# Optimization experiments

Measured on AMD Instinct MI355X. Metric: run time of the kernel, lower is better.

Reference implementation:

```python
import jax, jax.numpy as jnp
import numpy as np

B, N, FIN, FOUT, H = 8, 1024, 256, 256, 4
D = FOUT // H  # head_dim = 64
LN_EPS = 1e-5
NEG_INF = -1e9


def setup_inputs() -> dict:
    key = jax.random.key(0)
    k_x, k_adj, k_w, k_a = jax.random.split(key, 4)
    x = jax.random.normal(k_x, (B, N, FIN), dtype=jnp.float32)
    # sparse binary adjacency with self-loops (dense mask, as the module expects)
    adj = (jax.random.uniform(k_adj, (B, N, N)) < 0.05).astype(jnp.float32)
    adj = jnp.maximum(adj, jnp.eye(N, dtype=jnp.float32)[None])
    W = jax.random.normal(k_w, (FIN, FOUT), dtype=jnp.float32) * 0.02
    gamma = jnp.ones((FOUT,), dtype=jnp.float32)
    beta = jnp.zeros((FOUT,), dtype=jnp.float32)
    a = jax.random.normal(k_a, (2 * D,), dtype=jnp.float32) * 0.02
    return {"x": x, "adj_matrix": adj, "W": W, "gamma": gamma, "beta": beta, "a": a}


def reference(x, adj_matrix, W, gamma, beta, a):
    # h = LayerNorm(x @ W)
    h = jnp.einsum("bnf,fo->bno", x, W)
    mu = jnp.mean(h, axis=-1, keepdims=True)
    var = jnp.mean(jnp.square(h - mu), axis=-1, keepdims=True)
    h = (h - mu) * jax.lax.rsqrt(var + LN_EPS) * gamma + beta
    h = h.reshape(B, N, H, D)
    # a^T [h_i ; h_j] == a_src . h_i + a_dst . h_j  (exact decomposition of the
    # concat+Linear(2D->1) attention score, avoiding the O(B*N^2*H*2D) concat)
    a_src, a_dst = a[:D], a[D:]
    e_i = jnp.einsum("bnhd,d->bnh", h, a_src)  # term for node i (query)
    e_j = jnp.einsum("bnhd,d->bnh", h, a_dst)  # term for node j (key)
    e = e_i[:, :, None, :] + e_j[:, None, :, :]  # [B, N_i, N_j, H]
    e = jnp.where(e > 0, e, 0.2 * e)  # LeakyReLU(0.2)
    e = jnp.where(adj_matrix[..., None] == 0, NEG_INF, e)
    alpha = jax.nn.softmax(e, axis=2)  # softmax over neighbors j
    # dropout is identity in eval/reference mode
    h_out = jnp.einsum("bijh,bjhd->bihd", alpha, h)
    return h_out.reshape(B, N, FOUT)
```

## Files before the change

### kernel.cpp

```cpp
#include <hip/hip_runtime.h>
#include <hip/hip_bf16.h>

#define BB 8
#define NN 1024
#define FIN 256
#define FOUT 256
#define NH 4
#define DD 64
#define CAP 192

typedef short short8 __attribute__((ext_vector_type(8)));
typedef short short4v __attribute__((ext_vector_type(4)));
typedef float floatx4 __attribute__((ext_vector_type(4)));

__device__ __forceinline__ short f2bf(float f) {
    unsigned int u = __builtin_bit_cast(unsigned int, f);
    unsigned int r = (u + 0x7fffu + ((u >> 16) & 1u)) >> 16;
    return (short)r;
}

__global__ __launch_bounds__(256) void k_gemm(const float* __restrict__ x,
                                              const float* __restrict__ W,
                                              float* __restrict__ h) {
    __shared__ short As[64 * 40];
    __shared__ short Bt[64 * 40];
    const int m0 = blockIdx.x * 64;
    const int n0 = blockIdx.y * 64;
    const int t = threadIdx.x;
    const int w = t >> 6;
    const int lane = t & 63;
    const int quad = lane >> 4;
    const int l15 = lane & 15;

    floatx4 acc[4];
#pragma unroll
    for (int nt = 0; nt < 4; ++nt) acc[nt] = (floatx4)0.f;

    const int bn = t & 63;
    const int bkg = t >> 6;

    for (int k0 = 0; k0 < FIN; k0 += 32) {
#pragma unroll
        for (int q = 0; q < 2; ++q) {
            int lin = t * 4 + q * 1024;
            int m = lin >> 5, k = lin & 31;
            float4 v = *(const float4*)&x[(size_t)(m0 + m) * FIN + k0 + k];
            short4v s;
            s.x = f2bf(v.x); s.y = f2bf(v.y); s.z = f2bf(v.z); s.w = f2bf(v.w);
            *(short4v*)&As[m * 40 + k] = s;
        }
        {
            float f[8];
#pragma unroll
            for (int kk = 0; kk < 8; ++kk)
                f[kk] = W[(size_t)(k0 + bkg * 8 + kk) * FOUT + n0 + bn];
            short4v s0, s1;
            s0.x = f2bf(f[0]); s0.y = f2bf(f[1]); s0.z = f2bf(f[2]); s0.w = f2bf(f[3]);
            s1.x = f2bf(f[4]); s1.y = f2bf(f[5]); s1.z = f2bf(f[6]); s1.w = f2bf(f[7]);
            *(short4v*)&Bt[bn * 40 + bkg * 8]     = s0;
            *(short4v*)&Bt[bn * 40 + bkg * 8 + 4] = s1;
        }
        __syncthreads();
        short8 a = *(short8*)&As[(w * 16 + l15) * 40 + quad * 8];
#pragma unroll
        for (int nt = 0; nt < 4; ++nt) {
            short8 b = *(short8*)&Bt[(nt * 16 + l15) * 40 + quad * 8];
            acc[nt] = __builtin_amdgcn_mfma_f32_16x16x32_bf16(a, b, acc[nt], 0, 0, 0);
        }
        __syncthreads();
    }
#pragma unroll
    for (int nt = 0; nt < 4; ++nt)
#pragma unroll
        for (int reg = 0; reg < 4; ++reg)
            h[(size_t)(m0 + w * 16 + quad * 4 + reg) * FOUT + n0 + nt * 16 + l15] = acc[nt][reg];
}

__global__ __launch_bounds__(256) void k_ln(float* __restrict__ h,
                                            const float* __restrict__ gamma,
                                            const float* __restrict__ beta,
                                            const float* __restrict__ a,
                                            float* __restrict__ e_src,
                                            float* __restrict__ e_dst) {
    const int row = blockIdx.x;
    const int t = threadIdx.x;
    const size_t base = (size_t)row * FOUT;
    const int wave = t >> 6, lane = t & 63;
    __shared__ float red[8];

    float v = h[base + t];
    float s = v;
#pragma unroll
    for (int off = 32; off; off >>= 1) s += __shfl_xor(s, off);
    if (lane == 0) red[wave] = s;
    __syncthreads();
    float mean = (red[0] + red[1] + red[2] + red[3]) * (1.0f / 256.0f);
    float dv = v - mean;
    float q = dv * dv;
#pragma unroll
    for (int off = 32; off; off >>= 1) q += __shfl_xor(q, off);
    if (lane == 0) red[4 + wave] = q;
    __syncthreads();
    float var = (red[4] + red[5] + red[6] + red[7]) * (1.0f / 256.0f);
    float hn = dv * rsqrtf(var + 1e-5f) * gamma[t] + beta[t];
    h[base + t] = hn;

    float ps = hn * a[lane];
    float pd = hn * a[64 + lane];
#pragma unroll
    for (int off = 32; off; off >>= 1) {
        ps += __shfl_xor(ps, off);
        pd += __shfl_xor(pd, off);
    }
    if (lane == 0) {
        e_src[row * NH + wave] = ps;
        e_dst[row * NH + wave] = pd;
    }
}

__global__ __launch_bounds__(256) void k_attn(const float* __restrict__ h,
                                              const float* __restrict__ adj,
                                              const float* __restrict__ e_src,
                                              const float* __restrict__ e_dst,
                                              float* __restrict__ out) {
    __shared__ int cnt;
    __shared__ int jlist[CAP];
    __shared__ float4 wsl[CAP];
    __shared__ float accs[4][4][64];
    __shared__ float Ss[4][64];

    const int b = blockIdx.y;
    const int i = blockIdx.x;
    const int t = threadIdx.x;
    const float* hp   = h   + (size_t)b * NN * FOUT;
    const float* adjp = adj + ((size_t)b * NN + i) * NN;
    const float* edp  = e_dst + (size_t)b * NN * NH;

    const float4 esv = *(const float4*)&e_src[((size_t)b * NN + i) * NH];

    if (t == 0) cnt = 0;
    __syncthreads();

    float4 av = *(const float4*)&adjp[t * 4];
    float am[4] = {av.x, av.y, av.z, av.w};
#pragma unroll
    for (int q = 0; q < 4; ++q) {
        if (am[q] != 0.0f) {
            int j = t * 4 + q;
            int pos = atomicAdd(&cnt, 1);
            float4 ed = *(const float4*)&edp[(size_t)j * NH];
            float e0 = esv.x + ed.x, e1 = esv.y + ed.y, e2 = esv.z + ed.z, e3 = esv.w + ed.w;
            e0 = e0 > 0.f ? e0 : 0.2f * e0;
            e1 = e1 > 0.f ? e1 : 0.2f * e1;
            e2 = e2 > 0.f ? e2 : 0.2f * e2;
            e3 = e3 > 0.f ? e3 : 0.2f * e3;
            float4 w4;
            w4.x = __expf(e0); w4.y = __expf(e1); w4.z = __expf(e2); w4.w = __expf(e3);
            jlist[pos] = j;
            wsl[pos] = w4;
        }
    }
    __syncthreads();

    const int n = cnt;
    const int fg = t & 63;
    const int hh = fg >> 4;
    const int w = t >> 6;

    float4 acc = make_float4(0.f, 0.f, 0.f, 0.f);
    float S = 0.f;
    int p = w;
    while (p + 12 < n) {
        int jj[4]; float wv[4]; float4 hv[4];
#pragma unroll
        for (int q = 0; q < 4; ++q) jj[q] = jlist[p + q * 4];
#pragma unroll
        for (int q = 0; q < 4; ++q) {
            wv[q] = ((const float*)&wsl[p + q * 4])[hh];
            hv[q] = *(const float4*)&hp[(size_t)jj[q] * FOUT + fg * 4];
        }
#pragma unroll
        for (int q = 0; q < 4; ++q) {
            acc.x = fmaf(wv[q], hv[q].x, acc.x);
            acc.y = fmaf(wv[q], hv[q].y, acc.y);
            acc.z = fmaf(wv[q], hv[q].z, acc.z);
            acc.w = fmaf(wv[q], hv[q].w, acc.w);
            S += wv[q];
        }
        p += 16;
    }
    for (; p < n; p += 4) {
        int j = jlist[p];
        float wv = ((const float*)&wsl[p])[hh];
        float4 hv = *(const float4*)&hp[(size_t)j * FOUT + fg * 4];
        acc.x = fmaf(wv, hv.x, acc.x);
        acc.y = fmaf(wv, hv.y, acc.y);
        acc.z = fmaf(wv, hv.z, acc.z);
        acc.w = fmaf(wv, hv.w, acc.w);
        S += wv;
    }
    accs[w][0][fg] = acc.x; accs[w][1][fg] = acc.y;
    accs[w][2][fg] = acc.z; accs[w][3][fg] = acc.w;
    Ss[w][fg] = S;
    __syncthreads();

    if (t < 64) {
        float4 o = make_float4(0.f, 0.f, 0.f, 0.f);
        float St = 0.f;
#pragma unroll
        for (int q = 0; q < 4; ++q) {
            o.x += accs[q][0][t]; o.y += accs[q][1][t];
            o.z += accs[q][2][t]; o.w += accs[q][3][t];
            St += Ss[q][t];
        }
        float inv = 1.0f / St;
        o.x *= inv; o.y *= inv; o.z *= inv; o.w *= inv;
        *(float4*)&out[((size_t)b * NN + i) * FOUT + t * 4] = o;
    }
}

extern "C" void kernel_launch(void* const* d_in, const int* in_sizes, int n_in,
                              void* d_out, int out_size, void* d_ws, size_t ws_size,
                              hipStream_t stream) {
    const float* x     = (const float*)d_in[0];
    const float* adj   = (const float*)d_in[1];
    const float* W     = (const float*)d_in[2];
    const float* gamma = (const float*)d_in[3];
    const float* beta  = (const float*)d_in[4];
    const float* a     = (const float*)d_in[5];
    float* out = (float*)d_out;

    float* h     = (float*)d_ws;
    float* e_src = h + (size_t)BB * NN * FOUT;
    float* e_dst = e_src + (size_t)BB * NN * NH;

    k_gemm<<<dim3(128, 4), 256, 0, stream>>>(x, W, h);
    k_ln<<<dim3(BB * NN), 256, 0, stream>>>(h, gamma, beta, a, e_src, e_dst);
    k_attn<<<dim3(NN, BB), 256, 0, stream>>>(h, adj, e_src, e_dst, out);
}
```

Baseline: 128.5 us.

## Fuse GEMM with LayerNorm, store h as bf16, aggregate neighbor atomics per wave

Replaces the separate GEMM and LayerNorm kernels with one kernel that computes a 16-row tile against a pre-transposed bf16 W, applies LayerNorm and the attention score dot products in registers, and writes h as bf16. The attention kernel gathers bf16 neighbor rows, halving gather bytes. Per-element shared atomics become one ballot-based atomic per wave. Storing h in bf16 reduces precision of the aggregated output, and a small extra kernel transposes W each call.

```diff
diff --git a/kernel.cpp b/kernel.cpp
--- a/kernel.cpp
+++ b/kernel.cpp
@@ -6,7 +6,6 @@
 #define FIN 256
 #define FOUT 256
 #define NH 4
-#define DD 64
 #define CAP 192
 
 typedef short short8 __attribute__((ext_vector_type(8)));
@@ -18,107 +17,147 @@
     unsigned int r = (u + 0x7fffu + ((u >> 16) & 1u)) >> 16;
     return (short)r;
 }
-
-__global__ __launch_bounds__(256) void k_gemm(const float* __restrict__ x,
-                                              const float* __restrict__ W,
-                                              float* __restrict__ h) {
-    __shared__ short As[64 * 40];
-    __shared__ short Bt[64 * 40];
-    const int m0 = blockIdx.x * 64;
-    const int n0 = blockIdx.y * 64;
+__device__ __forceinline__ float bf2f(unsigned short s) {
+    return __builtin_bit_cast(float, (unsigned int)s << 16);
+}
+
+__global__ __launch_bounds__(256) void k_wt(const float* __restrict__ W,
+                                            unsigned short* __restrict__ Wt) {
+    __shared__ unsigned short ts[64][80];
+    const int k0 = blockIdx.x * 64, n0 = blockIdx.y * 64;
     const int t = threadIdx.x;
-    const int w = t >> 6;
-    const int lane = t & 63;
-    const int quad = lane >> 4;
-    const int l15 = lane & 15;
+#pragma unroll
+    for (int q = 0; q < 4; ++q) {
+        int lin = t + q * 256;
+        int r = lin >> 4, c4 = lin & 15;
+        float4 v = *(const float4*)&W[(size_t)(k0 + r) * FOUT + n0 + c4 * 4];
+        ts[c4 * 4 + 0][r] = (unsigned short)f2bf(v.x);
+        ts[c4 * 4 + 1][r] = (unsigned short)f2bf(v.y);
+        ts[c4 * 4 + 2][r] = (unsigned short)f2bf(v.z);
+        ts[c4 * 4 + 3][r] = (unsigned short)f2bf(v.w);
+    }
+    __syncthreads();
+#pragma unroll
+    for (int q = 0; q < 2; ++q) {
+        int lin = t + q * 256;
+        int row = lin >> 3, kg = lin & 7;
+        short8 s = *(short8*)&ts[row][kg * 8];
+        *(short8*)&Wt[(size_t)(n0 + row) * FIN + k0 + kg * 8] = s;
+    }
+}
+
+__global__ __launch_bounds__(256) void k_gemm_ln(const float* __restrict__ x,
+                                                 const unsigned short* __restrict__ Wt,
+                                                 const float* __restrict__ gamma,
+                                                 const float* __restrict__ beta,
+                                                 const float* __restrict__ a,
+                                                 unsigned short* __restrict__ hb,
+                                                 float* __restrict__ e_src,
+                                                 float* __restrict__ e_dst) {
+    __shared__ unsigned short As[16 * 264];
+    __shared__ float sumL[4][16], sqL[4][16];
+    const int m0 = blockIdx.x * 16;
+    const int t = threadIdx.x;
+    const int w = t >> 6, lane = t & 63, quad = lane >> 4, l15 = lane & 15;
+
+#pragma unroll
+    for (int q = 0; q < 4; ++q) {
+        int lin = t + q * 256;
+        int row = lin >> 6, c4 = lin & 63;
+        float4 v = *(const float4*)&x[(size_t)(m0 + row) * FIN + c4 * 4];
+        short4v s;
+        s.x = f2bf(v.x); s.y = f2bf(v.y); s.z = f2bf(v.z); s.w = f2bf(v.w);
+        *(short4v*)&As[row * 264 + c4 * 4] = s;
+    }
+    __syncthreads();
 
     floatx4 acc[4];
 #pragma unroll
     for (int nt = 0; nt < 4; ++nt) acc[nt] = (floatx4)0.f;
 
-    const int bn = t & 63;
-    const int bkg = t >> 6;
-
-    for (int k0 = 0; k0 < FIN; k0 += 32) {
-#pragma unroll
-        for (int q = 0; q < 2; ++q) {
-            int lin = t * 4 + q * 1024;
-            int m = lin >> 5, k = lin & 31;
-            float4 v = *(const float4*)&x[(size_t)(m0 + m) * FIN + k0 + k];
-            short4v s;
-            s.x = f2bf(v.x); s.y = f2bf(v.y); s.z = f2bf(v.z); s.w = f2bf(v.w);
-            *(short4v*)&As[m * 40 + k] = s;
-        }
-        {
-            float f[8];
-#pragma unroll
-            for (int kk = 0; kk < 8; ++kk)
-                f[kk] = W[(size_t)(k0 + bkg * 8 + kk) * FOUT + n0 + bn];
-            short4v s0, s1;
-            s0.x = f2bf(f[0]); s0.y = f2bf(f[1]); s0.z = f2bf(f[2]); s0.w = f2bf(f[3]);
-            s1.x = f2bf(f[4]); s1.y = f2bf(f[5]); s1.z = f2bf(f[6]); s1.w = f2bf(f[7]);
-            *(short4v*)&Bt[bn * 40 + bkg * 8]     = s0;
-            *(short4v*)&Bt[bn * 40 + bkg * 8 + 4] = s1;
-        }
-        __syncthreads();
-        short8 a = *(short8*)&As[(w * 16 + l15) * 40 + quad * 8];
+#pragma unroll
+    for (int ks = 0; ks < 8; ++ks) {
+        short8 af = *(short8*)&As[l15 * 264 + ks * 32 + quad * 8];
 #pragma unroll
         for (int nt = 0; nt < 4; ++nt) {
-            short8 b = *(short8*)&Bt[(nt * 16 + l15) * 40 + quad * 8];
-            acc[nt] = __builtin_amdgcn_mfma_f32_16x16x32_bf16(a, b, acc[nt], 0, 0, 0);
-        }
-        __syncthreads();
-    }
-#pragma unroll
-    for (int nt = 0; nt < 4; ++nt)
-#pragma unroll
-        for (int reg = 0; reg < 4; ++reg)
-            h[(size_t)(m0 + w * 16 + quad * 4 + reg) * FOUT + n0 + nt * 16 + l15] = acc[nt][reg];
-}
-
-__global__ __launch_bounds__(256) void k_ln(float* __restrict__ h,
-                                            const float* __restrict__ gamma,
-                                            const float* __restrict__ beta,
-                                            const float* __restrict__ a,
-                                            float* __restrict__ e_src,
-                                            float* __restrict__ e_dst) {
-    const int row = blockIdx.x;
-    const int t = threadIdx.x;
-    const size_t base = (size_t)row * FOUT;
-    const int wave = t >> 6, lane = t & 63;
-    __shared__ float red[8];
-
-    float v = h[base + t];
-    float s = v;
-#pragma unroll
-    for (int off = 32; off; off >>= 1) s += __shfl_xor(s, off);
-    if (lane == 0) red[wave] = s;
-    __syncthreads();
-    float mean = (red[0] + red[1] + red[2] + red[3]) * (1.0f / 256.0f);
-    float dv = v - mean;
-    float q = dv * dv;
-#pragma unroll
-    for (int off = 32; off; off >>= 1) q += __shfl_xor(q, off);
-    if (lane == 0) red[4 + wave] = q;
-    __syncthreads();
-    float var = (red[4] + red[5] + red[6] + red[7]) * (1.0f / 256.0f);
-    float hn = dv * rsqrtf(var + 1e-5f) * gamma[t] + beta[t];
-    h[base + t] = hn;
-
-    float ps = hn * a[lane];
-    float pd = hn * a[64 + lane];
-#pragma unroll
-    for (int off = 32; off; off >>= 1) {
-        ps += __shfl_xor(ps, off);
-        pd += __shfl_xor(pd, off);
-    }
-    if (lane == 0) {
-        e_src[row * NH + wave] = ps;
-        e_dst[row * NH + wave] = pd;
-    }
-}
-
-__global__ __launch_bounds__(256) void k_attn(const float* __restrict__ h,
+            short8 bf = *(const short8*)&Wt[(size_t)((w * 4 + nt) * 16 + l15) * FIN + ks * 32 + quad * 8];
+            acc[nt] = __builtin_amdgcn_mfma_f32_16x16x32_bf16(af, bf, acc[nt], 0, 0, 0);
+        }
+    }
+
+    float rs[4], rq[4];
+#pragma unroll
+    for (int reg = 0; reg < 4; ++reg) {
+        float s = 0.f, q2 = 0.f;
+#pragma unroll
+        for (int nt = 0; nt < 4; ++nt) { float v = acc[nt][reg]; s += v; q2 = fmaf(v, v, q2); }
+#pragma unroll
+        for (int off = 1; off < 16; off <<= 1) { s += __shfl_xor(s, off); q2 += __shfl_xor(q2, off); }
+        rs[reg] = s; rq[reg] = q2;
+    }
+    if (l15 == 0) {
+#pragma unroll
+        for (int reg = 0; reg < 4; ++reg) {
+            sumL[w][quad * 4 + reg] = rs[reg];
+            sqL[w][quad * 4 + reg] = rq[reg];
+        }
+    }
+    __syncthreads();
+
+    float g[4], bt[4], as_[4], ad_[4];
+#pragma unroll
+    for (int nt = 0; nt < 4; ++nt) {
+        int col = w * 64 + nt * 16 + l15;
+        g[nt] = gamma[col]; bt[nt] = beta[col];
+        int d = nt * 16 + l15;
+        as_[nt] = a[d]; ad_[nt] = a[64 + d];
+    }
+
+    float pes[4], ped[4];
+#pragma unroll
+    for (int reg = 0; reg < 4; ++reg) {
+        int row = quad * 4 + reg;
+        float mean = (sumL[0][row] + sumL[1][row] + sumL[2][row] + sumL[3][row]) * (1.f / 256.f);
+        float msq  = (sqL[0][row] + sqL[1][row] + sqL[2][row] + sqL[3][row]) * (1.f / 256.f);
+        float inv = rsqrtf(msq - mean * mean + 1e-5f);
+        float es = 0.f, ed = 0.f;
+#pragma unroll
+        for (int nt = 0; nt < 4; ++nt) {
+            float hn = (acc[nt][reg] - mean) * inv * g[nt] + bt[nt];
+            As[row * 264 + w * 64 + nt * 16 + l15] = (unsigned short)f2bf(hn);
+            es = fmaf(hn, as_[nt], es);
+            ed = fmaf(hn, ad_[nt], ed);
+        }
+        pes[reg] = es; ped[reg] = ed;
+    }
+#pragma unroll
+    for (int reg = 0; reg < 4; ++reg) {
+#pragma unroll
+        for (int off = 1; off < 16; off <<= 1) {
+            pes[reg] += __shfl_xor(pes[reg], off);
+            ped[reg] += __shfl_xor(ped[reg], off);
+        }
+    }
+    if (l15 == 0) {
+#pragma unroll
+        for (int reg = 0; reg < 4; ++reg) {
+            int rowg = m0 + quad * 4 + reg;
+            e_src[rowg * NH + w] = pes[reg];
+            e_dst[rowg * NH + w] = ped[reg];
+        }
+    }
+    __syncthreads();
+
+#pragma unroll
+    for (int q = 0; q < 2; ++q) {
+        int lin = t + q * 256;
+        int row = lin >> 5, cg = lin & 31;
+        short8 s = *(short8*)&As[row * 264 + cg * 8];
+        *(short8*)&hb[(size_t)(m0 + row) * FOUT + cg * 8] = s;
+    }
+}
+
+__global__ __launch_bounds__(256) void k_attn(const unsigned short* __restrict__ hb,
                                               const float* __restrict__ adj,
                                               const float* __restrict__ e_src,
                                               const float* __restrict__ e_dst,
@@ -132,10 +171,11 @@
     const int b = blockIdx.y;
     const int i = blockIdx.x;
     const int t = threadIdx.x;
-    const float* hp   = h   + (size_t)b * NN * FOUT;
+    const int lane = t & 63;
+    const int w = t >> 6;
+    const unsigned short* hp = hb + (size_t)b * NN * FOUT;
     const float* adjp = adj + ((size_t)b * NN + i) * NN;
     const float* edp  = e_dst + (size_t)b * NN * NH;
-
     const float4 esv = *(const float4*)&e_src[((size_t)b * NN + i) * NH];
 
     if (t == 0) cnt = 0;
@@ -145,9 +185,14 @@
     float am[4] = {av.x, av.y, av.z, av.w};
 #pragma unroll
     for (int q = 0; q < 4; ++q) {
-        if (am[q] != 0.0f) {
+        bool nz = (am[q] != 0.0f);
+        unsigned long long mask = __ballot(nz);
+        int basew = 0;
+        if (lane == 0) basew = mask ? atomicAdd(&cnt, __popcll(mask)) : 0;
+        basew = __shfl(basew, 0);
+        if (nz) {
+            int pos = basew + __popcll(mask & ((1ull << lane) - 1ull));
             int j = t * 4 + q;
-            int pos = atomicAdd(&cnt, 1);
             float4 ed = *(const float4*)&edp[(size_t)j * NH];
             float e0 = esv.x + ed.x, e1 = esv.y + ed.y, e2 = esv.z + ed.z, e3 = esv.w + ed.w;
             e0 = e0 > 0.f ? e0 : 0.2f * e0;
@@ -163,42 +208,44 @@
     __syncthreads();
 
     const int n = cnt;
-    const int fg = t & 63;
+    const int fg = lane;
     const int hh = fg >> 4;
-    const int w = t >> 6;
-
     float4 acc = make_float4(0.f, 0.f, 0.f, 0.f);
     float S = 0.f;
-    int p = w;
-    while (p + 12 < n) {
-        int jj[4]; float wv[4]; float4 hv[4];
-#pragma unroll
-        for (int q = 0; q < 4; ++q) jj[q] = jlist[p + q * 4];
+
+    int idx = w;
+    while (idx + 12 < n) {
+        int jj[4]; float wv[4]; short4v hv[4];
 #pragma unroll
         for (int q = 0; q < 4; ++q) {
-            wv[q] = ((const float*)&wsl[p + q * 4])[hh];
-            hv[q] = *(const float4*)&hp[(size_t)jj[q] * FOUT + fg * 4];
-        }
+            int p = idx + 4 * q;
+            jj[q] = jlist[p];
+            wv[q] = ((const float*)&wsl[p])[hh];
+        }
+#pragma unroll
+        for (int q = 0; q < 4; ++q)
+            hv[q] = *(const short4v*)&hp[(size_t)jj[q] * FOUT + fg * 4];
 #pragma unroll
         for (int q = 0; q < 4; ++q) {
-            acc.x = fmaf(wv[q], hv[q].x, acc.x);
-            acc.y = fmaf(wv[q], hv[q].y, acc.y);
-            acc.z = fmaf(wv[q], hv[q].z, acc.z);
-            acc.w = fmaf(wv[q], hv[q].w, acc.w);
+            acc.x = fmaf(wv[q], bf2f((unsigned short)hv[q].x), acc.x);
+            acc.y = fmaf(wv[q], bf2f((unsigned short)hv[q].y), acc.y);
+            acc.z = fmaf(wv[q], bf2f((unsigned short)hv[q].z), acc.z);
+            acc.w = fmaf(wv[q], bf2f((unsigned short)hv[q].w), acc.w);
             S += wv[q];
         }
-        p += 16;
-    }
-    for (; p < n; p += 4) {
-        int j = jlist[p];
-        float wv = ((const float*)&wsl[p])[hh];
-        float4 hv = *(const float4*)&hp[(size_t)j * FOUT + fg * 4];
-        acc.x = fmaf(wv, hv.x, acc.x);
-        acc.y = fmaf(wv, hv.y, acc.y);
-        acc.z = fmaf(wv, hv.z, acc.z);
-        acc.w = fmaf(wv, hv.w, acc.w);
+        idx += 16;
+    }
+    for (; idx < n; idx += 4) {
+        int j = jlist[idx];
+        float wv = ((const float*)&wsl[idx])[hh];
+        short4v hv = *(const short4v*)&hp[(size_t)j * FOUT + fg * 4];
+        acc.x = fmaf(wv, bf2f((unsigned short)hv.x), acc.x);
+        acc.y = fmaf(wv, bf2f((unsigned short)hv.y), acc.y);
+        acc.z = fmaf(wv, bf2f((unsigned short)hv.z), acc.z);
+        acc.w = fmaf(wv, bf2f((unsigned short)hv.w), acc.w);
         S += wv;
     }
+
     accs[w][0][fg] = acc.x; accs[w][1][fg] = acc.y;
     accs[w][2][fg] = acc.z; accs[w][3][fg] = acc.w;
     Ss[w][fg] = S;
@@ -230,11 +277,12 @@
     const float* a     = (const float*)d_in[5];
     float* out = (float*)d_out;
 
-    float* h     = (float*)d_ws;
-    float* e_src = h + (size_t)BB * NN * FOUT;
+    unsigned short* Wt = (unsigned short*)d_ws;
+    unsigned short* hb = Wt + (size_t)FIN * FOUT;
+    float* e_src = (float*)(hb + (size_t)BB * NN * FOUT);
     float* e_dst = e_src + (size_t)BB * NN * NH;
 
-    k_gemm<<<dim3(128, 4), 256, 0, stream>>>(x, W, h);
-    k_ln<<<dim3(BB * NN), 256, 0, stream>>>(h, gamma, beta, a, e_src, e_dst);
-    k_attn<<<dim3(NN, BB), 256, 0, stream>>>(h, adj, e_src, e_dst, out);
-}
+    k_wt<<<dim3(4, 4), 256, 0, stream>>>(W, Wt);
+    k_gemm_ln<<<dim3(512), 256, 0, stream>>>(x, Wt, gamma, beta, a, hb, e_src, e_dst);
+    k_attn<<<dim3(NN, BB), 256, 0, stream>>>(hb, adj, e_src, e_dst, out);
+}
```

Measured after the change: 123.0 us. -4.3%, faster.
